# Kernel optimization log

Measured on AMD Instinct MI355X. Metric: run time of the kernel, lower is better.

## Reference

```python
import jax, jax.numpy as jnp
import numpy as np

N_SRC = 50000
N_EDGES = 150000
D_IN = 512
D_OUT = 512

def setup_inputs() -> dict:
    key = jax.random.key(0)
    k1, k2, k3, k4, k5 = jax.random.split(key, 5)
    src_h = jax.random.normal(k1, (N_SRC, D_IN), dtype=jnp.float32)
    W = jax.random.normal(k2, (D_OUT, D_IN), dtype=jnp.float32) * (1.0 / np.sqrt(D_IN))
    b = jax.random.normal(k3, (D_OUT,), dtype=jnp.float32) * 0.01
    src_idx = jax.random.randint(k4, (N_EDGES,), 0, N_SRC, dtype=jnp.int64) if jax.config.jax_enable_x64 else jax.random.randint(k4, (N_EDGES,), 0, N_SRC, dtype=jnp.int32)
    dst_idx = jax.random.randint(k5, (N_EDGES,), 0, N_SRC, dtype=src_idx.dtype)
    return {"src_h": src_h, "W": W, "b": b, "src_idx": src_idx, "dst_idx": dst_idx, "n_dst": N_SRC}

def reference(src_h, W, b, src_idx, dst_idx, n_dst):
    # message passing: copy src feature to each edge, sum into dst nodes
    msgs = src_h[src_idx]                                  # [E, D_in]
    agg = jax.ops.segment_sum(msgs, dst_idx, num_segments=n_dst)  # [N_dst, D_in]
    # dense linear (apply_linear == 'linear' -> no relu)
    return agg @ W.T + b                                   # [N_dst, D_out]
```

## Files before the change

### kernel.cpp

```cpp
#include <hip/hip_runtime.h>
#include <hip/hip_bf16.h>

#define D 512
#define BM 128
#define BN 128
#define BK 32
#define SB 512

typedef __attribute__((ext_vector_type(8))) short bf16x8;
typedef __attribute__((ext_vector_type(4))) float f32x4;

__device__ __forceinline__ unsigned short bf16_rne(float f) {
    union { float f; unsigned u; } v; v.f = f;
    return (unsigned short)((v.u + 0x7FFFu + ((v.u >> 16) & 1u)) >> 16);
}

__device__ __forceinline__ void gload16(const void* g, void* l) {
    __builtin_amdgcn_global_load_lds(
        (const __attribute__((address_space(1))) void*)g,
        (__attribute__((address_space(3))) void*)l,
        16, 0, 0);
}

__device__ __forceinline__ void facc(float4& a, const float4 v) {
    a.x += v.x; a.y += v.y; a.z += v.z; a.w += v.w;
}

__global__ __launch_bounds__(256) void prep_kernel(const float* __restrict__ W,
                                                   unsigned short* __restrict__ wb,
                                                   const int* __restrict__ dst, int E,
                                                   int* __restrict__ cnt) {
    const int b = blockIdx.x;
    const int t = threadIdx.x;
    if (b < 512) {
        const int i = b * 256 + t;
        float2 v = ((const float2*)W)[i];
        unsigned r = ((unsigned)bf16_rne(v.x)) | (((unsigned)bf16_rne(v.y)) << 16);
        ((unsigned*)wb)[i] = r;
    } else {
        const int e = (b - 512) * 256 + t;
        if (e < E) atomicAdd(&cnt[dst[e]], 1);
    }
}


__global__ __launch_bounds__(256) void scan_reduce_kernel(const int* __restrict__ cnt, int M,
                                                          int* __restrict__ bsum) {
    const int t = threadIdx.x;
    const int i0 = blockIdx.x * SB + t * 2;
    int v = 0;
    if (i0 < M)     v += cnt[i0];
    if (i0 + 1 < M) v += cnt[i0 + 1];
    #pragma unroll
    for (int o = 32; o > 0; o >>= 1) v += __shfl_down(v, o, 64);
    __shared__ int ws_[4];
    if ((t & 63) == 0) ws_[t >> 6] = v;
    __syncthreads();
    if (t == 0) bsum[blockIdx.x] = ws_[0] + ws_[1] + ws_[2] + ws_[3];
}

__global__ __launch_bounds__(256) void scan_final_kernel(int* __restrict__ cnt, int M,
                                                         const int* __restrict__ bsum, int NB,
                                                         int* __restrict__ offsets) {
    __shared__ int sb[256];
    __shared__ int s[256];
    const int t = threadIdx.x;

    int bv = (t < NB) ? bsum[t] : 0;
    sb[t] = bv;
    __syncthreads();
    #pragma unroll
    for (int o = 1; o < 256; o <<= 1) {
        int u = (t >= o) ? sb[t - o] : 0;
        __syncthreads();
        sb[t] += u;
        __syncthreads();
    }
    if (blockIdx.x == 0 && t == 255) offsets[M] = sb[255];
    const int bexcl = (blockIdx.x > 0) ? sb[blockIdx.x - 1] : 0;

    const int base = blockIdx.x * SB + t * 2;
    int a = (base < M) ? cnt[base] : 0;
    int b = (base + 1 < M) ? cnt[base + 1] : 0;
    const int tsum = a + b;
    s[t] = tsum;
    __syncthreads();
    #pragma unroll
    for (int o = 1; o < 256; o <<= 1) {
        int u = (t >= o) ? s[t - o] : 0;
        __syncthreads();
        s[t] += u;
        __syncthreads();
    }
    const int excl = s[t] - tsum + bexcl;
    if (base < M)     { offsets[base] = excl;         cnt[base] = excl; }
    if (base + 1 < M) { offsets[base + 1] = excl + a; cnt[base + 1] = excl + a; }
}

__global__ __launch_bounds__(256) void sort_kernel(const int* __restrict__ src,
                                                   const int* __restrict__ dst, int E,
                                                   int* __restrict__ cursor,
                                                   int* __restrict__ sorted_src) {
    int e = blockIdx.x * 256 + threadIdx.x;
    if (e < E) {
        int pos = atomicAdd(&cursor[dst[e]], 1);
        sorted_src[pos] = src[e];
    }
}

__global__ __launch_bounds__(256) void agg_kernel(const float* __restrict__ src_h,
                                                  const int* __restrict__ offsets,
                                                  const int* __restrict__ sorted_src,
                                                  unsigned short* __restrict__ aggb,
                                                  int M) {
    const int wv = threadIdx.x >> 6;
    const int lane = threadIdx.x & 63;
    const int d = blockIdx.x * 4 + wv;
    if (d >= M) return;
    const int beg = offsets[d];
    const int end = offsets[d + 1];
    const float4* rb = (const float4*)src_h;

    float4 a0 = {0.f, 0.f, 0.f, 0.f};
    float4 a1 = {0.f, 0.f, 0.f, 0.f};
    int e = beg;

    for (; e + 4 <= end; e += 4) {
        const int s0 = sorted_src[e];
        const int s1 = sorted_src[e + 1];
        const int s2 = sorted_src[e + 2];
        const int s3 = sorted_src[e + 3];
        float4 v00 = rb[(size_t)s0 * 128 + lane];
        float4 v01 = rb[(size_t)s0 * 128 + 64 + lane];
        float4 v10 = rb[(size_t)s1 * 128 + lane];
        float4 v11 = rb[(size_t)s1 * 128 + 64 + lane];
        float4 v20 = rb[(size_t)s2 * 128 + lane];
        float4 v21 = rb[(size_t)s2 * 128 + 64 + lane];
        float4 v30 = rb[(size_t)s3 * 128 + lane];
        float4 v31 = rb[(size_t)s3 * 128 + 64 + lane];
        facc(a0, v00); facc(a1, v01);
        facc(a0, v10); facc(a1, v11);
        facc(a0, v20); facc(a1, v21);
        facc(a0, v30); facc(a1, v31);
    }
    if (e + 2 <= end) {
        const int s0 = sorted_src[e];
        const int s1 = sorted_src[e + 1];
        float4 v00 = rb[(size_t)s0 * 128 + lane];
        float4 v01 = rb[(size_t)s0 * 128 + 64 + lane];
        float4 v10 = rb[(size_t)s1 * 128 + lane];
        float4 v11 = rb[(size_t)s1 * 128 + 64 + lane];
        facc(a0, v00); facc(a1, v01);
        facc(a0, v10); facc(a1, v11);
        e += 2;
    }
    if (e < end) {
        const int s0 = sorted_src[e];
        float4 v00 = rb[(size_t)s0 * 128 + lane];
        float4 v01 = rb[(size_t)s0 * 128 + 64 + lane];
        facc(a0, v00); facc(a1, v01);
    }

    ushort4 o0, o1;
    o0.x = bf16_rne(a0.x); o0.y = bf16_rne(a0.y);
    o0.z = bf16_rne(a0.z); o0.w = bf16_rne(a0.w);
    o1.x = bf16_rne(a1.x); o1.y = bf16_rne(a1.y);
    o1.z = bf16_rne(a1.z); o1.w = bf16_rne(a1.w);
    *(ushort4*)(aggb + (size_t)d * D + lane * 4) = o0;
    *(ushort4*)(aggb + (size_t)d * D + 256 + lane * 4) = o1;
}

__global__ __launch_bounds__(256) void gemm_kernel(const unsigned short* __restrict__ A,
                                                   const unsigned short* __restrict__ B,
                                                   const float* __restrict__ bias,
                                                   float* __restrict__ out,
                                                   int M, int MB_tiles) {
    __shared__ __align__(16) unsigned short As[2 * BM * BK];
    __shared__ __align__(16) unsigned short Bs[2 * BN * BK];

    const int L = blockIdx.x;
    const int mb = (L >> 5) * 8 + (L & 7);
    const int nb = (L >> 3) & 3;
    if (mb >= MB_tiles) return;
    const int m0 = mb * BM;
    const int n0 = nb * BN;

    const int t = threadIdx.x;
    const int lane = t & 63;
    const int wave = t >> 6;
    const int wm = wave >> 1;
    const int wn = wave & 1;
    const int quad = lane >> 4;
    const int lr = lane & 15;

    const int srow = t >> 2;
    const int scol = ((t & 3) ^ ((t >> 3) & 3)) * 8;
    const int arow0 = min(m0 + srow, M - 1);
    const int arow1 = min(m0 + 64 + srow, M - 1);
    const int brow0 = n0 + srow;
    const int brow1 = n0 + 64 + srow;
    const unsigned short* ag0 = A + (size_t)arow0 * D + scol;
    const unsigned short* ag1 = A + (size_t)arow1 * D + scol;
    const unsigned short* bg0 = B + (size_t)brow0 * D + scol;
    const unsigned short* bg1 = B + (size_t)brow1 * D + scol;

    const int fsw = (quad ^ ((lr >> 1) & 3)) * 8;

    f32x4 acc[4][4] = {};

    gload16(ag0, As + t * 8);
    gload16(ag1, As + 2048 + t * 8);
    gload16(bg0, Bs + t * 8);
    gload16(bg1, Bs + 2048 + t * 8);
    asm volatile("s_waitcnt vmcnt(0)" ::: "memory");
    __builtin_amdgcn_s_barrier();

    for (int kt = 0; kt < 16; ++kt) {
        const int cur = (kt & 1) * 4096;
        const int nxt = 4096 - cur;
        if (kt + 1 < 16) {
            const int k0n = (kt + 1) * BK;
            gload16(ag0 + k0n, As + nxt + t * 8);
            gload16(ag1 + k0n, As + nxt + 2048 + t * 8);
            gload16(bg0 + k0n, Bs + nxt + t * 8);
            gload16(bg1 + k0n, Bs + nxt + 2048 + t * 8);
        }

        bf16x8 af[4], bfr[4];
        #pragma unroll
        for (int i = 0; i < 4; ++i) {
            af[i]  = *(const bf16x8*)&As[cur + (wm * 64 + i * 16 + lr) * BK + fsw];
            bfr[i] = *(const bf16x8*)&Bs[cur + (wn * 64 + i * 16 + lr) * BK + fsw];
        }
        #pragma unroll
        for (int i = 0; i < 4; ++i)
            #pragma unroll
            for (int j = 0; j < 4; ++j)
                acc[i][j] = __builtin_amdgcn_mfma_f32_16x16x32_bf16(bfr[j], af[i], acc[i][j], 0, 0, 0);

        if (kt + 1 < 16) {
            asm volatile("s_waitcnt vmcnt(0)" ::: "memory");
            __builtin_amdgcn_s_barrier();
        }
    }

    #pragma unroll
    for (int i = 0; i < 4; ++i) {
        const int row = m0 + wm * 64 + i * 16 + lr;
        if (row >= M) continue;
        #pragma unroll
        for (int j = 0; j < 4; ++j) {
            const int colb = n0 + wn * 64 + j * 16 + quad * 4;
            const float4 bv = *(const float4*)(bias + colb);
            float4 o;
            o.x = acc[i][j][0] + bv.x;
            o.y = acc[i][j][1] + bv.y;
            o.z = acc[i][j][2] + bv.z;
            o.w = acc[i][j][3] + bv.w;
            *(float4*)(out + (size_t)row * D + colb) = o;
        }
    }
}

extern "C" void kernel_launch(void* const* d_in, const int* in_sizes, int n_in,
                              void* d_out, int out_size, void* d_ws, size_t ws_size,
                              hipStream_t stream) {
    const float* src_h = (const float*)d_in[0];
    const float* W     = (const float*)d_in[1];
    const float* b     = (const float*)d_in[2];
    const int*   si    = (const int*)d_in[3];
    const int*   di    = (const int*)d_in[4];
    const int M = in_sizes[0] / D;
    const int E = in_sizes[3];
    const int NB = (M + SB - 1) / SB;

    char* ws = (char*)d_ws;
    unsigned short* aggb = (unsigned short*)ws;
    unsigned short* wb   = (unsigned short*)(ws + 51200000);
    int* offsets         = (int*)(ws + 51724288);
    int* cnt             = (int*)(ws + 51924480);
    int* ssrc            = (int*)(ws + 52124480);
    int* bsum            = (int*)(ws + 52724480);

    hipMemsetAsync(cnt, 0, (size_t)M * sizeof(int), stream);
    const int HB = (E + 255) / 256;
    prep_kernel<<<dim3(512 + HB), 256, 0, stream>>>(W, wb, di, E, cnt);
    scan_reduce_kernel<<<dim3(NB), 256, 0, stream>>>(cnt, M, bsum);
    scan_final_kernel<<<dim3(NB), 256, 0, stream>>>(cnt, M, bsum, NB, offsets);
    sort_kernel<<<dim3((E + 255) / 256), 256, 0, stream>>>(si, di, E, cnt, ssrc);
    agg_kernel<<<dim3((M + 3) / 4), 256, 0, stream>>>(src_h, offsets, ssrc, aggb, M);

    const int MB_tiles = (M + BM - 1) / BM;
    const int ngrid = ((MB_tiles + 7) / 8) * 32;
    gemm_kernel<<<dim3(ngrid), 256, 0, stream>>>(aggb, wb, b, (float*)d_out, M, MB_tiles);
}
```

Baseline: 274.6 us.

## Apply linear before aggregation and gather bf16 transformed rows

Uses linearity to reorder the computation: the GEMM now runs on src_h (converting fp32 to bf16 in registers while staging into LDS) to produce Y = src_h·W^T in bf16. A gather kernel then sums the Y rows of each destination's sorted edges and adds the bias. The gather now reads 1 KB bf16 rows instead of 2 KB fp32 rows, and the bf16 aggregate buffer round trip goes away. In exchange the GEMM must load fp32 A through registers rather than with direct-to-LDS loads, and it rounds Y to bf16 before summation, which changes the rounding behaviour.

```diff
diff --git a/kernel.cpp b/kernel.cpp
--- a/kernel.cpp
+++ b/kernel.cpp
@@ -15,15 +15,17 @@
     return (unsigned short)((v.u + 0x7FFFu + ((v.u >> 16) & 1u)) >> 16);
 }
 
+__device__ __forceinline__ float bf2f(short s) {
+    union { unsigned u; float f; } v;
+    v.u = ((unsigned)(unsigned short)s) << 16;
+    return v.f;
+}
+
 __device__ __forceinline__ void gload16(const void* g, void* l) {
     __builtin_amdgcn_global_load_lds(
         (const __attribute__((address_space(1))) void*)g,
         (__attribute__((address_space(3))) void*)l,
         16, 0, 0);
-}
-
-__device__ __forceinline__ void facc(float4& a, const float4 v) {
-    a.x += v.x; a.y += v.y; a.z += v.z; a.w += v.w;
 }
 
 __global__ __launch_bounds__(256) void prep_kernel(const float* __restrict__ W,
@@ -108,72 +110,9 @@
     }
 }
 
-__global__ __launch_bounds__(256) void agg_kernel(const float* __restrict__ src_h,
-                                                  const int* __restrict__ offsets,
-                                                  const int* __restrict__ sorted_src,
-                                                  unsigned short* __restrict__ aggb,
-                                                  int M) {
-    const int wv = threadIdx.x >> 6;
-    const int lane = threadIdx.x & 63;
-    const int d = blockIdx.x * 4 + wv;
-    if (d >= M) return;
-    const int beg = offsets[d];
-    const int end = offsets[d + 1];
-    const float4* rb = (const float4*)src_h;
-
-    float4 a0 = {0.f, 0.f, 0.f, 0.f};
-    float4 a1 = {0.f, 0.f, 0.f, 0.f};
-    int e = beg;
-
-    for (; e + 4 <= end; e += 4) {
-        const int s0 = sorted_src[e];
-        const int s1 = sorted_src[e + 1];
-        const int s2 = sorted_src[e + 2];
-        const int s3 = sorted_src[e + 3];
-        float4 v00 = rb[(size_t)s0 * 128 + lane];
-        float4 v01 = rb[(size_t)s0 * 128 + 64 + lane];
-        float4 v10 = rb[(size_t)s1 * 128 + lane];
-        float4 v11 = rb[(size_t)s1 * 128 + 64 + lane];
-        float4 v20 = rb[(size_t)s2 * 128 + lane];
-        float4 v21 = rb[(size_t)s2 * 128 + 64 + lane];
-        float4 v30 = rb[(size_t)s3 * 128 + lane];
-        float4 v31 = rb[(size_t)s3 * 128 + 64 + lane];
-        facc(a0, v00); facc(a1, v01);
-        facc(a0, v10); facc(a1, v11);
-        facc(a0, v20); facc(a1, v21);
-        facc(a0, v30); facc(a1, v31);
-    }
-    if (e + 2 <= end) {
-        const int s0 = sorted_src[e];
-        const int s1 = sorted_src[e + 1];
-        float4 v00 = rb[(size_t)s0 * 128 + lane];
-        float4 v01 = rb[(size_t)s0 * 128 + 64 + lane];
-        float4 v10 = rb[(size_t)s1 * 128 + lane];
-        float4 v11 = rb[(size_t)s1 * 128 + 64 + lane];
-        facc(a0, v00); facc(a1, v01);
-        facc(a0, v10); facc(a1, v11);
-        e += 2;
-    }
-    if (e < end) {
-        const int s0 = sorted_src[e];
-        float4 v00 = rb[(size_t)s0 * 128 + lane];
-        float4 v01 = rb[(size_t)s0 * 128 + 64 + lane];
-        facc(a0, v00); facc(a1, v01);
-    }
-
-    ushort4 o0, o1;
-    o0.x = bf16_rne(a0.x); o0.y = bf16_rne(a0.y);
-    o0.z = bf16_rne(a0.z); o0.w = bf16_rne(a0.w);
-    o1.x = bf16_rne(a1.x); o1.y = bf16_rne(a1.y);
-    o1.z = bf16_rne(a1.z); o1.w = bf16_rne(a1.w);
-    *(ushort4*)(aggb + (size_t)d * D + lane * 4) = o0;
-    *(ushort4*)(aggb + (size_t)d * D + 256 + lane * 4) = o1;
-}
-
-__global__ __launch_bounds__(256) void gemm_kernel(const unsigned short* __restrict__ A,
+__global__ __launch_bounds__(256) void gemm_kernel(const float* __restrict__ A,
                                                    const unsigned short* __restrict__ B,
-                                                   const float* __restrict__ bias,
-                                                   float* __restrict__ out,
+                                                   unsigned short* __restrict__ Y,
                                                    int M, int MB_tiles) {
     __shared__ __align__(16) unsigned short As[2 * BM * BK];
     __shared__ __align__(16) unsigned short Bs[2 * BN * BK];
@@ -197,31 +136,43 @@
     const int scol = ((t & 3) ^ ((t >> 3) & 3)) * 8;
     const int arow0 = min(m0 + srow, M - 1);
     const int arow1 = min(m0 + 64 + srow, M - 1);
-    const int brow0 = n0 + srow;
-    const int brow1 = n0 + 64 + srow;
-    const unsigned short* ag0 = A + (size_t)arow0 * D + scol;
-    const unsigned short* ag1 = A + (size_t)arow1 * D + scol;
-    const unsigned short* bg0 = B + (size_t)brow0 * D + scol;
-    const unsigned short* bg1 = B + (size_t)brow1 * D + scol;
+    const float* ag0 = A + (size_t)arow0 * D + scol;
+    const float* ag1 = A + (size_t)arow1 * D + scol;
+    const unsigned short* bg0 = B + (size_t)(n0 + srow) * D + scol;
+    const unsigned short* bg1 = B + (size_t)(n0 + 64 + srow) * D + scol;
 
     const int fsw = (quad ^ ((lr >> 1) & 3)) * 8;
 
     f32x4 acc[4][4] = {};
 
-    gload16(ag0, As + t * 8);
-    gload16(ag1, As + 2048 + t * 8);
+    float4 p00, p01, p10, p11;
+
+    p00 = *(const float4*)(ag0);     p01 = *(const float4*)(ag0 + 4);
+    p10 = *(const float4*)(ag1);     p11 = *(const float4*)(ag1 + 4);
     gload16(bg0, Bs + t * 8);
     gload16(bg1, Bs + 2048 + t * 8);
-    asm volatile("s_waitcnt vmcnt(0)" ::: "memory");
-    __builtin_amdgcn_s_barrier();
+    {
+        union { bf16x8 v; unsigned short u[8]; } w0, w1;
+        w0.u[0] = bf16_rne(p00.x); w0.u[1] = bf16_rne(p00.y);
+        w0.u[2] = bf16_rne(p00.z); w0.u[3] = bf16_rne(p00.w);
+        w0.u[4] = bf16_rne(p01.x); w0.u[5] = bf16_rne(p01.y);
+        w0.u[6] = bf16_rne(p01.z); w0.u[7] = bf16_rne(p01.w);
+        w1.u[0] = bf16_rne(p10.x); w1.u[1] = bf16_rne(p10.y);
+        w1.u[2] = bf16_rne(p10.z); w1.u[3] = bf16_rne(p10.w);
+        w1.u[4] = bf16_rne(p11.x); w1.u[5] = bf16_rne(p11.y);
+        w1.u[6] = bf16_rne(p11.z); w1.u[7] = bf16_rne(p11.w);
+        *(bf16x8*)&As[t * 8] = w0.v;
+        *(bf16x8*)&As[2048 + t * 8] = w1.v;
+    }
+    __syncthreads();
 
     for (int kt = 0; kt < 16; ++kt) {
         const int cur = (kt & 1) * 4096;
         const int nxt = 4096 - cur;
         if (kt + 1 < 16) {
             const int k0n = (kt + 1) * BK;
-            gload16(ag0 + k0n, As + nxt + t * 8);
-            gload16(ag1 + k0n, As + nxt + 2048 + t * 8);
+            p00 = *(const float4*)(ag0 + k0n); p01 = *(const float4*)(ag0 + k0n + 4);
+            p10 = *(const float4*)(ag1 + k0n); p11 = *(const float4*)(ag1 + k0n + 4);
             gload16(bg0 + k0n, Bs + nxt + t * 8);
             gload16(bg1 + k0n, Bs + nxt + 2048 + t * 8);
         }
@@ -239,8 +190,18 @@
                 acc[i][j] = __builtin_amdgcn_mfma_f32_16x16x32_bf16(bfr[j], af[i], acc[i][j], 0, 0, 0);
 
         if (kt + 1 < 16) {
-            asm volatile("s_waitcnt vmcnt(0)" ::: "memory");
-            __builtin_amdgcn_s_barrier();
+            union { bf16x8 v; unsigned short u[8]; } w0, w1;
+            w0.u[0] = bf16_rne(p00.x); w0.u[1] = bf16_rne(p00.y);
+            w0.u[2] = bf16_rne(p00.z); w0.u[3] = bf16_rne(p00.w);
+            w0.u[4] = bf16_rne(p01.x); w0.u[5] = bf16_rne(p01.y);
+            w0.u[6] = bf16_rne(p01.z); w0.u[7] = bf16_rne(p01.w);
+            w1.u[0] = bf16_rne(p10.x); w1.u[1] = bf16_rne(p10.y);
+            w1.u[2] = bf16_rne(p10.z); w1.u[3] = bf16_rne(p10.w);
+            w1.u[4] = bf16_rne(p11.x); w1.u[5] = bf16_rne(p11.y);
+            w1.u[6] = bf16_rne(p11.z); w1.u[7] = bf16_rne(p11.w);
+            *(bf16x8*)&As[nxt + t * 8] = w0.v;
+            *(bf16x8*)&As[nxt + 2048 + t * 8] = w1.v;
+            __syncthreads();
         }
     }
 
@@ -251,15 +212,81 @@
         #pragma unroll
         for (int j = 0; j < 4; ++j) {
             const int colb = n0 + wn * 64 + j * 16 + quad * 4;
-            const float4 bv = *(const float4*)(bias + colb);
-            float4 o;
-            o.x = acc[i][j][0] + bv.x;
-            o.y = acc[i][j][1] + bv.y;
-            o.z = acc[i][j][2] + bv.z;
-            o.w = acc[i][j][3] + bv.w;
-            *(float4*)(out + (size_t)row * D + colb) = o;
+            ushort4 o;
+            o.x = bf16_rne(acc[i][j][0]);
+            o.y = bf16_rne(acc[i][j][1]);
+            o.z = bf16_rne(acc[i][j][2]);
+            o.w = bf16_rne(acc[i][j][3]);
+            *(ushort4*)(Y + (size_t)row * D + colb) = o;
         }
     }
+}
+
+__global__ __launch_bounds__(256) void gather_kernel(const unsigned short* __restrict__ Y,
+                                                     const int* __restrict__ offsets,
+                                                     const int* __restrict__ sorted_src,
+                                                     const float* __restrict__ bias,
+                                                     float* __restrict__ out, int M) {
+    const int wv = threadIdx.x >> 6;
+    const int lane = threadIdx.x & 63;
+    const int d = blockIdx.x * 4 + wv;
+    if (d >= M) return;
+    const int beg = offsets[d];
+    const int end = offsets[d + 1];
+    const bf16x8* yb = (const bf16x8*)Y;
+
+    const float4 b0 = *(const float4*)(bias + lane * 8);
+    const float4 b1 = *(const float4*)(bias + lane * 8 + 4);
+    float a0 = b0.x, a1 = b0.y, a2 = b0.z, a3 = b0.w;
+    float a4 = b1.x, a5 = b1.y, a6 = b1.z, a7 = b1.w;
+
+    int e = beg;
+    for (; e + 4 <= end; e += 4) {
+        const int s0 = sorted_src[e];
+        const int s1 = sorted_src[e + 1];
+        const int s2 = sorted_src[e + 2];
+        const int s3 = sorted_src[e + 3];
+        bf16x8 r0 = yb[(size_t)s0 * 64 + lane];
+        bf16x8 r1 = yb[(size_t)s1 * 64 + lane];
+        bf16x8 r2 = yb[(size_t)s2 * 64 + lane];
+        bf16x8 r3 = yb[(size_t)s3 * 64 + lane];
+        a0 += bf2f(r0[0]) + bf2f(r1[0]) + bf2f(r2[0]) + bf2f(r3[0]);
+        a1 += bf2f(r0[1]) + bf2f(r1[1]) + bf2f(r2[1]) + bf2f(r3[1]);
+        a2 += bf2f(r0[2]) + bf2f(r1[2]) + bf2f(r2[2]) + bf2f(r3[2]);
+        a3 += bf2f(r0[3]) + bf2f(r1[3]) + bf2f(r2[3]) + bf2f(r3[3]);
+        a4 += bf2f(r0[4]) + bf2f(r1[4]) + bf2f(r2[4]) + bf2f(r3[4]);
+        a5 += bf2f(r0[5]) + bf2f(r1[5]) + bf2f(r2[5]) + bf2f(r3[5]);
+        a6 += bf2f(r0[6]) + bf2f(r1[6]) + bf2f(r2[6]) + bf2f(r3[6]);
+        a7 += bf2f(r0[7]) + bf2f(r1[7]) + bf2f(r2[7]) + bf2f(r3[7]);
+    }
+    if (e + 2 <= end) {
+        const int s0 = sorted_src[e];
+        const int s1 = sorted_src[e + 1];
+        bf16x8 r0 = yb[(size_t)s0 * 64 + lane];
+        bf16x8 r1 = yb[(size_t)s1 * 64 + lane];
+        a0 += bf2f(r0[0]) + bf2f(r1[0]);
+        a1 += bf2f(r0[1]) + bf2f(r1[1]);
+        a2 += bf2f(r0[2]) + bf2f(r1[2]);
+        a3 += bf2f(r0[3]) + bf2f(r1[3]);
+        a4 += bf2f(r0[4]) + bf2f(r1[4]);
+        a5 += bf2f(r0[5]) + bf2f(r1[5]);
+        a6 += bf2f(r0[6]) + bf2f(r1[6]);
+        a7 += bf2f(r0[7]) + bf2f(r1[7]);
+        e += 2;
+    }
+    if (e < end) {
+        const int s0 = sorted_src[e];
+        bf16x8 r0 = yb[(size_t)s0 * 64 + lane];
+        a0 += bf2f(r0[0]); a1 += bf2f(r0[1]);
+        a2 += bf2f(r0[2]); a3 += bf2f(r0[3]);
+        a4 += bf2f(r0[4]); a5 += bf2f(r0[5]);
+        a6 += bf2f(r0[6]); a7 += bf2f(r0[7]);
+    }
+
+    float4 o0 = {a0, a1, a2, a3};
+    float4 o1 = {a4, a5, a6, a7};
+    *(float4*)(out + (size_t)d * D + lane * 8) = o0;
+    *(float4*)(out + (size_t)d * D + lane * 8 + 4) = o1;
 }
 
 extern "C" void kernel_launch(void* const* d_in, const int* in_sizes, int n_in,
@@ -275,7 +302,7 @@
     const int NB = (M + SB - 1) / SB;
 
     char* ws = (char*)d_ws;
-    unsigned short* aggb = (unsigned short*)ws;
+    unsigned short* Y    = (unsigned short*)ws;
     unsigned short* wb   = (unsigned short*)(ws + 51200000);
     int* offsets         = (int*)(ws + 51724288);
     int* cnt             = (int*)(ws + 51924480);
@@ -285,12 +312,14 @@
     hipMemsetAsync(cnt, 0, (size_t)M * sizeof(int), stream);
     const int HB = (E + 255) / 256;
     prep_kernel<<<dim3(512 + HB), 256, 0, stream>>>(W, wb, di, E, cnt);
+
+    const int MB_tiles = (M + BM - 1) / BM;
+    const int ngrid = ((MB_tiles + 7) / 8) * 32;
+    gemm_kernel<<<dim3(ngrid), 256, 0, stream>>>(src_h, wb, Y, M, MB_tiles);
+
     scan_reduce_kernel<<<dim3(NB), 256, 0, stream>>>(cnt, M, bsum);
     scan_final_kernel<<<dim3(NB), 256, 0, stream>>>(cnt, M, bsum, NB, offsets);
     sort_kernel<<<dim3((E + 255) / 256), 256, 0, stream>>>(si, di, E, cnt, ssrc);
-    agg_kernel<<<dim3((M + 3) / 4), 256, 0, stream>>>(src_h, offsets, ssrc, aggb, M);
-
-    const int MB_tiles = (M + BM - 1) / BM;
-    const int ngrid = ((MB_tiles + 7) / 8) * 32;
-    gemm_kernel<<<dim3(ngrid), 256, 0, stream>>>(aggb, wb, b, (float*)d_out, M, MB_tiles);
-}
+    gather_kernel<<<dim3((M + 3) / 4), 256, 0, stream>>>(Y, offsets, ssrc, b,
+                                                         (float*)d_out, M);
+}
```

Result: slower. 290.8 us (+5.9%).
